# Performance work log

Measured on AMD Instinct MI355X. Metric: run time of the kernel, lower is better.

The kernel has to match this reference:

```python
import jax, jax.numpy as jnp
import numpy as np

H = W = 256          # render / reference image size (module crops ref to 256x256)
TS = 4               # texture_size in the module
EYE_DIST, ELEV, AZIM = 2.732, 0.0, np.pi / 2  # fixed azimuth (orig: uniform(0,360))
EPS = 1e-8


def _look_at(verts, eye):
    # neural_renderer look_at: at=origin, up=+y
    up = jnp.array([0.0, 1.0, 0.0], dtype=verts.dtype)
    z = -eye / jnp.linalg.norm(eye)
    x = jnp.cross(up, z)
    x = x / jnp.linalg.norm(x)
    y = jnp.cross(z, x)
    R = jnp.stack([x, y, z], axis=0)  # rows = camera axes
    return (verts - eye) @ R.T


def _cross2(u, v):
    return u[..., 0] * v[..., 1] - u[..., 1] * v[..., 0]


def _render(vertices, faces, textures):
    # Orthographic (perspective=False), ambient-only lighting -> color == texture sample.
    eye = jnp.array([EYE_DIST * np.cos(ELEV) * np.sin(AZIM),
                     EYE_DIST * np.sin(ELEV),
                     -EYE_DIST * np.cos(ELEV) * np.cos(AZIM)], dtype=vertices.dtype)
    v = _look_at(vertices[0], eye)            # [V,3] camera space
    fv = v[faces[0]]                          # [F,3,3]
    a, b, c = fv[:, 0, :2], fv[:, 1, :2], fv[:, 2, :2]  # [F,2] screen-space verts
    zf = fv[..., 2]                           # [F,3] per-vertex depth

    # pixel centers in NDC, y flipped (image row 0 = top)
    xs = (jnp.arange(W, dtype=vertices.dtype) + 0.5) / W * 2.0 - 1.0
    ys = 1.0 - (jnp.arange(H, dtype=vertices.dtype) + 0.5) / H * 2.0
    P = jnp.stack(jnp.meshgrid(xs, ys, indexing='xy'), -1).reshape(-1, 2)  # [HW,2]
    Pq = P[:, None, :]                        # [HW,1,2]

    denom = _cross2(b - a, c - a)             # [F] signed 2*area
    w0 = _cross2((c - b)[None], Pq - b[None])  # [HW,F] edge functions
    w1 = _cross2((a - c)[None], Pq - c[None])
    w2 = _cross2((b - a)[None], Pq - a[None])
    s = jnp.sign(denom)[None]
    nondeg = (jnp.abs(denom) > EPS)[None]
    inside = (w0 * s >= 0) & (w1 * s >= 0) & (w2 * s >= 0) & nondeg
    d = jnp.where(jnp.abs(denom) > EPS, denom, 1.0)[None]
    w0, w1, w2 = w0 / d, w1 / d, w2 / d       # normalized barycentrics
    depth = w0 * zf[None, :, 0] + w1 * zf[None, :, 1] + w2 * zf[None, :, 2]  # [HW,F]
    visible = inside & (depth > 0)

    # z-buffer: nearest visible face per pixel
    zbuf = jnp.where(visible, depth, jnp.inf)
    best = jnp.argmin(zbuf, axis=1)           # [HW]
    hit = jnp.take_along_axis(visible, best[:, None], 1)[:, 0]
    bw = jnp.stack([jnp.take_along_axis(wi, best[:, None], 1)[:, 0]
                    for wi in (w0, w1, w2)], axis=-1)  # [HW,3]

    # sample face texture cube [TS,TS,TS] by barycentric coords (nearest)
    ti = jnp.clip(jnp.round(bw * (TS - 1)).astype(jnp.int32), 0, TS - 1)
    color = textures[0][best, ti[:, 0], ti[:, 1], ti[:, 2]]  # [HW,3]
    img = jnp.where(hit[:, None], color, jnp.zeros_like(color)).reshape(H, W, 3)
    return jnp.transpose(img, (2, 0, 1))[None]  # [1,3,H,W]


def setup_inputs() -> dict:
    key = jax.random.key(0)
    k1, k2, k3, k4 = jax.random.split(key, 4)
    V, F = 642, 512
    verts = jax.random.normal(k1, (1, V, 3), jnp.float32)
    verts = verts / (jnp.linalg.norm(verts, axis=-1, keepdims=True) + 1e-6)  # unit sphere
    faces = jax.random.randint(k2, (1, F, 3), 0, V, jnp.int32)
    textures = jax.random.normal(k3, (1, F, TS, TS, TS, 3), jnp.float32)
    image_ref = jax.random.uniform(k4, (1, 3, H, W), jnp.float32)
    return {"vertices": verts, "textures": textures, "image_ref": image_ref, "faces": faces}


def reference(vertices, textures, image_ref, faces):
    image = _render(vertices, faces, jnp.tanh(textures))
    return jnp.sum((image - image_ref) ** 2)
```

## Files before the change

### kernel.cpp

```cpp
#include <hip/hip_runtime.h>
#include <math.h>

#define NFACE 512
#define NVERT 642
#define NPIX  (256 * 256)
#define DXS   (2.0f / 256.0f)

#define EYEX 2.732f
#define EYEZ (-1.6728675276352845e-16f)
#define CC0  (6.123233995736766e-17f)

__global__ __launch_bounds__(256) void render_loss(
    const float* __restrict__ verts,
    const int*   __restrict__ faces,
    const float* __restrict__ tex,
    const float* __restrict__ ref,
    float* __restrict__ out)
{
    __shared__ float  sverts[NVERT * 3];
    __shared__ float4 sf0[NFACE];
    __shared__ float4 sf1[NFACE];
    __shared__ float4 flist[NFACE];
    __shared__ float4 plist[NFACE][3];
    __shared__ int   fcnt, pcnt;
    __shared__ unsigned Mu;
    __shared__ float wsum[4];

    int tid = threadIdx.x;
    if (tid == 0) { fcnt = 0; pcnt = 0; Mu = 0x7f800000u; }

    for (int k = tid; k < NVERT * 3; k += 256) sverts[k] = verts[k];
    __syncthreads();

    int tileX = (blockIdx.x & 15) << 4;
    int tileY = (blockIdx.x >> 4) << 4;
    float xlo = (tileX + 0.5f)  * DXS - 1.0f;
    float xhi = (tileX + 15.5f) * DXS - 1.0f;
    float yhi = 1.0f - (tileY + 0.5f)  * DXS;
    float ylo = 1.0f - (tileY + 15.5f) * DXS;

    float rc[2][9];
    int   rcls[2];
    float rdmn[2];
#pragma unroll
    for (int it = 0; it < 2; ++it) {
        int f = tid + it * 256;
        rcls[it] = 0;
        float vx[3], vy[3], vz[3];
#pragma unroll
        for (int k = 0; k < 3; ++k) {
            int vi = faces[f * 3 + k];
            float px = sverts[vi * 3 + 0];
            float py = sverts[vi * 3 + 1];
            float pz = sverts[vi * 3 + 2];
            float dx = px - EYEX;
            float dz = pz - EYEZ;
            vx[k] = CC0 * dx + dz;
            vy[k] = py;
            vz[k] = -dx + CC0 * dz;
        }
        float ax = vx[0], ay = vy[0];
        float bx = vx[1], by = vy[1];
        float cx = vx[2], cy = vy[2];
        float denom = (bx - ax) * (cy - ay) - (by - ay) * (cx - ax);
        if (fabsf(denom) <= 1e-8f) continue;

        float si = 1.0f / denom;
        float e0x = cx - bx, e0y = cy - by;
        float e1x = ax - cx, e1y = ay - cy;
        float e2x = bx - ax, e2y = by - ay;
        float A0 = e0x * si, B0 = -e0y * si, C0 = (e0y * bx - e0x * by) * si;
        float A1 = e1x * si, B1 = -e1y * si, C1 = (e1y * cx - e1x * cy) * si;
        float A2 = e2x * si, B2 = -e2y * si, C2 = (e2y * ax - e2x * ay) * si;
        float DA = A0 * vz[0] + A1 * vz[1] + A2 * vz[2];
        float DB = B0 * vz[0] + B1 * vz[1] + B2 * vz[2];
        float DC = C0 * vz[0] + C1 * vz[1] + C2 * vz[2];

        sf0[f] = make_float4(A0, B0, C0, A1);
        sf1[f] = make_float4(B1, C1, DA, DB);

        float bxmn = fminf(fminf(ax, bx), cx), bxmx = fmaxf(fmaxf(ax, bx), cx);
        float bymn = fminf(fminf(ay, by), cy), bymx = fmaxf(fmaxf(ay, by), cy);
        if ((bxmn > xhi + 1e-5f) | (bxmx < xlo - 1e-5f) |
            (bymn > yhi + 1e-5f) | (bymx < ylo - 1e-5f)) continue;

        float wmx[3], wmn[3], mg[3];
        float As[3] = {A0, A1, A2}, Bs[3] = {B0, B1, B2}, Cs[3] = {C0, C1, C2};
#pragma unroll
        for (int k = 0; k < 3; ++k) {
            float t1 = As[k] * ylo, t2 = As[k] * yhi;
            float u1 = Bs[k] * xlo, u2 = Bs[k] * xhi;
            wmx[k] = fmaxf(t1, t2) + fmaxf(u1, u2) + Cs[k];
            wmn[k] = fminf(t1, t2) + fminf(u1, u2) + Cs[k];
            mg[k]  = (fabsf(As[k]) + fabsf(Bs[k]) + fabsf(Cs[k])) * 2e-6f;
        }
        if ((wmx[0] < -mg[0]) | (wmx[1] < -mg[1]) | (wmx[2] < -mg[2])) continue;
        bool full = (wmn[0] > mg[0]) & (wmn[1] > mg[1]) & (wmn[2] > mg[2]);

        float t1 = DA * ylo, t2 = DA * yhi;
        float u1 = DB * xlo, u2 = DB * xhi;
        float dmx = fmaxf(t1, t2) + fmaxf(u1, u2) + DC;
        float dmn = fminf(t1, t2) + fminf(u1, u2) + DC;
        float md  = (fabsf(DA) + fabsf(DB) + fabsf(DC)) * 2e-6f + 1e-4f;
        rdmn[it] = dmn - md;
        rcls[it] = full ? 1 : 2;
        rc[it][0] = A0; rc[it][1] = B0; rc[it][2] = C0;
        rc[it][3] = A1; rc[it][4] = B1; rc[it][5] = C1;
        rc[it][6] = DA; rc[it][7] = DB; rc[it][8] = DC;
        if (full) atomicMin(&Mu, __float_as_uint(dmx + md));
    }
    __syncthreads();

    float M = __uint_as_float(Mu);
#pragma unroll
    for (int it = 0; it < 2; ++it) {
        if (rcls[it] == 0 || rdmn[it] > M) continue;
        int f = tid + it * 256;
        float fb = __uint_as_float((unsigned)f);
        if (rcls[it] == 1) {
            int s = atomicAdd(&fcnt, 1);
            flist[s] = make_float4(rc[it][6], rc[it][7], rc[it][8], fb);
        } else {
            int s = atomicAdd(&pcnt, 1);
            plist[s][0] = make_float4(rc[it][0], rc[it][1], rc[it][2], rc[it][3]);
            plist[s][1] = make_float4(rc[it][4], rc[it][5], rc[it][6], rc[it][7]);
            plist[s][2] = make_float4(rc[it][8], fb, 0.f, 0.f);
        }
    }
    __syncthreads();
    int fc = fcnt, pc = pcnt;

    int i = tileX + (tid & 15);
    int j = tileY + (tid >> 4);
    float Px = (i + 0.5f) * DXS - 1.0f;
    float Py = 1.0f - (j + 0.5f) * DXS;

    unsigned best = 0xFFFFFFFFu;
    int k = 0;
    for (; k + 4 <= fc; k += 4) {
        float4 ra = flist[k + 0], rb = flist[k + 1];
        float4 rcc = flist[k + 2], rd = flist[k + 3];
        float da = fmaf(ra.x, Py, fmaf(ra.y, Px, ra.z));
        float db = fmaf(rb.x, Py, fmaf(rb.y, Px, rb.z));
        float dc = fmaf(rcc.x, Py, fmaf(rcc.y, Px, rcc.z));
        float dd = fmaf(rd.x, Py, fmaf(rd.y, Px, rd.z));
        unsigned ca = (__float_as_uint(da) & 0xFFFFFE00u) | __float_as_uint(ra.w);
        unsigned cb = (__float_as_uint(db) & 0xFFFFFE00u) | __float_as_uint(rb.w);
        unsigned cc = (__float_as_uint(dc) & 0xFFFFFE00u) | __float_as_uint(rcc.w);
        unsigned cd = (__float_as_uint(dd) & 0xFFFFFE00u) | __float_as_uint(rd.w);
        ca = ca < cb ? ca : cb;
        cc = cc < cd ? cc : cd;
        ca = ca < cc ? ca : cc;
        best = best < ca ? best : ca;
    }
    for (; k < fc; ++k) {
        float4 r = flist[k];
        float dep = fmaf(r.x, Py, fmaf(r.y, Px, r.z));
        unsigned cand = (__float_as_uint(dep) & 0xFFFFFE00u) | __float_as_uint(r.w);
        best = best < cand ? best : cand;
    }
    k = 0;
    for (; k + 2 <= pc; k += 2) {
        float4 a0 = plist[k][0], a1 = plist[k][1], a2 = plist[k][2];
        float4 b0 = plist[k+1][0], b1 = plist[k+1][1], b2 = plist[k+1][2];
        float aw0 = fmaf(a0.x, Py, fmaf(a0.y, Px, a0.z));
        float aw1 = fmaf(a0.w, Py, fmaf(a1.x, Px, a1.y));
        float aw2 = 1.0f - aw0 - aw1;
        float adp = fmaf(a1.z, Py, fmaf(a1.w, Px, a2.x));
        float amn = fminf(fminf(aw0, aw1), aw2);
        unsigned ac = (__float_as_uint(adp) & 0xFFFFFE00u) | __float_as_uint(a2.y);
        ac = (amn >= 0.f) ? ac : 0xFFFFFFFFu;
        float bw0 = fmaf(b0.x, Py, fmaf(b0.y, Px, b0.z));
        float bw1 = fmaf(b0.w, Py, fmaf(b1.x, Px, b1.y));
        float bw2 = 1.0f - bw0 - bw1;
        float bdp = fmaf(b1.z, Py, fmaf(b1.w, Px, b2.x));
        float bmn = fminf(fminf(bw0, bw1), bw2);
        unsigned bc = (__float_as_uint(bdp) & 0xFFFFFE00u) | __float_as_uint(b2.y);
        bc = (bmn >= 0.f) ? bc : 0xFFFFFFFFu;
        ac = ac < bc ? ac : bc;
        best = best < ac ? best : ac;
    }
    for (; k < pc; ++k) {
        float4 q0 = plist[k][0], q1 = plist[k][1], q2 = plist[k][2];
        float w0  = fmaf(q0.x, Py, fmaf(q0.y, Px, q0.z));
        float w1  = fmaf(q0.w, Py, fmaf(q1.x, Px, q1.y));
        float w2  = 1.0f - w0 - w1;
        float dep = fmaf(q1.z, Py, fmaf(q1.w, Px, q2.x));
        float mn  = fminf(fminf(w0, w1), w2);
        unsigned cand = (__float_as_uint(dep) & 0xFFFFFE00u) | __float_as_uint(q2.y);
        cand = (mn >= 0.f) ? cand : 0xFFFFFFFFu;
        best = best < cand ? best : cand;
    }

    int p = j * 256 + i;
    float col0 = 0.f, col1 = 0.f, col2 = 0.f;
    if (best != 0xFFFFFFFFu) {
        int bf = (int)(best & 511u);
        float4 q0 = sf0[bf];
        float4 q1 = sf1[bf];
        float w0 = fmaf(q0.x, Py, fmaf(q0.y, Px, q0.z));
        float w1 = fmaf(q0.w, Py, fmaf(q1.x, Px, q1.y));
        float w2 = 1.0f - w0 - w1;
        int t0 = (int)rintf(w0 * 3.0f); t0 = t0 < 0 ? 0 : (t0 > 3 ? 3 : t0);
        int t1 = (int)rintf(w1 * 3.0f); t1 = t1 < 0 ? 0 : (t1 > 3 ? 3 : t1);
        int t2 = (int)rintf(w2 * 3.0f); t2 = t2 < 0 ? 0 : (t2 > 3 ? 3 : t2);
        const float* tp = tex + ((((bf * 4 + t0) * 4 + t1) * 4 + t2) * 3);
        col0 = tanhf(tp[0]);
        col1 = tanhf(tp[1]);
        col2 = tanhf(tp[2]);
    }
    float r0 = ref[0 * NPIX + p];
    float r1 = ref[1 * NPIX + p];
    float r2 = ref[2 * NPIX + p];
    float e0 = col0 - r0, e1 = col1 - r1, e2 = col2 - r2;
    float loss = e0 * e0 + e1 * e1 + e2 * e2;

    for (int off = 32; off > 0; off >>= 1)
        loss += __shfl_down(loss, off, 64);
    int lane = tid & 63;
    int wid  = tid >> 6;
    if (lane == 0) wsum[wid] = loss;
    __syncthreads();
    if (tid == 0)
        atomicAdd(out, wsum[0] + wsum[1] + wsum[2] + wsum[3]);
}

extern "C" void kernel_launch(void* const* d_in, const int* in_sizes, int n_in,
                              void* d_out, int out_size, void* d_ws, size_t ws_size,
                              hipStream_t stream) {
    const float* verts = (const float*)d_in[0];
    const float* tex   = (const float*)d_in[1];
    const float* ref   = (const float*)d_in[2];
    const int*   faces = (const int*)d_in[3];
    float* out = (float*)d_out;

    hipMemsetAsync(out, 0, sizeof(float), stream);
    render_loss<<<256, 256, 0, stream>>>(verts, faces, tex, ref, out);
}
```

Baseline: 17.67 us.

## Split face lists across waves and compute four pixel rows per thread

Each wave now handles a quarter of the candidate face lists. Each thread evaluates four vertically adjacent pixels per face, sharing the Px-dependent terms, and the four per-wave minima are merged through shared memory. Per-thread LDS reads and loop trip counts drop by about a factor of four, at the cost of an extra barrier and a shared reduction buffer. The third edge coefficients are also derived algebraically from the first two, and the partial-face list is split into separate arrays.

```diff
diff --git a/kernel.cpp b/kernel.cpp
--- a/kernel.cpp
+++ b/kernel.cpp
@@ -21,7 +21,10 @@
     __shared__ float4 sf0[NFACE];
     __shared__ float4 sf1[NFACE];
     __shared__ float4 flist[NFACE];
-    __shared__ float4 plist[NFACE][3];
+    __shared__ float4 pl0[NFACE];
+    __shared__ float4 pl1[NFACE];
+    __shared__ float2 pld[NFACE];
+    __shared__ unsigned marr[4][256];
     __shared__ int   fcnt, pcnt;
     __shared__ unsigned Mu;
     __shared__ float wsum[4];
@@ -71,7 +74,7 @@
         float e2x = bx - ax, e2y = by - ay;
         float A0 = e0x * si, B0 = -e0y * si, C0 = (e0y * bx - e0x * by) * si;
         float A1 = e1x * si, B1 = -e1y * si, C1 = (e1y * cx - e1x * cy) * si;
-        float A2 = e2x * si, B2 = -e2y * si, C2 = (e2y * ax - e2x * ay) * si;
+        float A2 = -(A0 + A1), B2 = -(B0 + B1), C2 = 1.0f - C0 - C1;
         float DA = A0 * vz[0] + A1 * vz[1] + A2 * vz[2];
         float DB = B0 * vz[0] + B1 * vz[1] + B2 * vz[2];
         float DC = C0 * vz[0] + C1 * vz[1] + C2 * vz[2];
@@ -122,84 +125,94 @@
             flist[s] = make_float4(rc[it][6], rc[it][7], rc[it][8], fb);
         } else {
             int s = atomicAdd(&pcnt, 1);
-            plist[s][0] = make_float4(rc[it][0], rc[it][1], rc[it][2], rc[it][3]);
-            plist[s][1] = make_float4(rc[it][4], rc[it][5], rc[it][6], rc[it][7]);
-            plist[s][2] = make_float4(rc[it][8], fb, 0.f, 0.f);
+            pl0[s] = make_float4(rc[it][0], rc[it][1], rc[it][2], rc[it][3]);
+            pl1[s] = make_float4(rc[it][4], rc[it][5], rc[it][6], rc[it][7]);
+            pld[s] = make_float2(rc[it][8], fb);
         }
     }
     __syncthreads();
     int fc = fcnt, pc = pcnt;
+
+    int lane = tid & 63;
+    int w    = tid >> 6;
+    int col   = lane & 15;
+    int rbase = (lane >> 4) << 2;
+    float Px  = (tileX + col + 0.5f) * DXS - 1.0f;
+    float Py0 = 1.0f - (tileY + rbase + 0.5f) * DXS;
+
+    unsigned pk0 = 0xFFFFFFFFu, pk1 = 0xFFFFFFFFu;
+    unsigned pk2 = 0xFFFFFFFFu, pk3 = 0xFFFFFFFFu;
+
+#pragma unroll 2
+    for (int k = w; k < fc; k += 4) {
+        float4 r = flist[k];
+        float td = fmaf(r.y, Px, r.z);
+        float d0 = fmaf(r.x, Py0, td);
+        float d1 = fmaf(r.x, Py0 - DXS, td);
+        float d2 = fmaf(r.x, Py0 - 2.0f * DXS, td);
+        float d3 = fmaf(r.x, Py0 - 3.0f * DXS, td);
+        unsigned fb = __float_as_uint(r.w);
+        unsigned c0 = (__float_as_uint(d0) & 0xFFFFFE00u) | fb;
+        unsigned c1 = (__float_as_uint(d1) & 0xFFFFFE00u) | fb;
+        unsigned c2 = (__float_as_uint(d2) & 0xFFFFFE00u) | fb;
+        unsigned c3 = (__float_as_uint(d3) & 0xFFFFFE00u) | fb;
+        pk0 = pk0 < c0 ? pk0 : c0;
+        pk1 = pk1 < c1 ? pk1 : c1;
+        pk2 = pk2 < c2 ? pk2 : c2;
+        pk3 = pk3 < c3 ? pk3 : c3;
+    }
+
+#pragma unroll 2
+    for (int k = w; k < pc; k += 4) {
+        float4 q0 = pl0[k];
+        float4 q1 = pl1[k];
+        float2 qd = pld[k];
+        float t0 = fmaf(q0.y, Px, q0.z);
+        float t1 = fmaf(q1.x, Px, q1.y);
+        float td = fmaf(q1.w, Px, qd.x);
+        unsigned fb = __float_as_uint(qd.y);
+#pragma unroll
+        for (int q = 0; q < 4; ++q) {
+            float Py = Py0 - (float)q * DXS;
+            float w0 = fmaf(q0.x, Py, t0);
+            float w1 = fmaf(q0.w, Py, t1);
+            float w2 = 1.0f - w0 - w1;
+            float dp = fmaf(q1.z, Py, td);
+            float mn = fminf(fminf(w0, w1), w2);
+            unsigned cd = (__float_as_uint(dp) & 0xFFFFFE00u) | fb;
+            cd = (mn >= 0.f) ? cd : 0xFFFFFFFFu;
+            if (q == 0) pk0 = pk0 < cd ? pk0 : cd;
+            if (q == 1) pk1 = pk1 < cd ? pk1 : cd;
+            if (q == 2) pk2 = pk2 < cd ? pk2 : cd;
+            if (q == 3) pk3 = pk3 < cd ? pk3 : cd;
+        }
+    }
+
+    marr[w][(rbase + 0) * 16 + col] = pk0;
+    marr[w][(rbase + 1) * 16 + col] = pk1;
+    marr[w][(rbase + 2) * 16 + col] = pk2;
+    marr[w][(rbase + 3) * 16 + col] = pk3;
+    __syncthreads();
+    unsigned best = marr[0][tid];
+    unsigned m1 = marr[1][tid];
+    unsigned m2 = marr[2][tid];
+    unsigned m3 = marr[3][tid];
+    best = best < m1 ? best : m1;
+    best = best < m2 ? best : m2;
+    best = best < m3 ? best : m3;
 
     int i = tileX + (tid & 15);
     int j = tileY + (tid >> 4);
-    float Px = (i + 0.5f) * DXS - 1.0f;
-    float Py = 1.0f - (j + 0.5f) * DXS;
-
-    unsigned best = 0xFFFFFFFFu;
-    int k = 0;
-    for (; k + 4 <= fc; k += 4) {
-        float4 ra = flist[k + 0], rb = flist[k + 1];
-        float4 rcc = flist[k + 2], rd = flist[k + 3];
-        float da = fmaf(ra.x, Py, fmaf(ra.y, Px, ra.z));
-        float db = fmaf(rb.x, Py, fmaf(rb.y, Px, rb.z));
-        float dc = fmaf(rcc.x, Py, fmaf(rcc.y, Px, rcc.z));
-        float dd = fmaf(rd.x, Py, fmaf(rd.y, Px, rd.z));
-        unsigned ca = (__float_as_uint(da) & 0xFFFFFE00u) | __float_as_uint(ra.w);
-        unsigned cb = (__float_as_uint(db) & 0xFFFFFE00u) | __float_as_uint(rb.w);
-        unsigned cc = (__float_as_uint(dc) & 0xFFFFFE00u) | __float_as_uint(rcc.w);
-        unsigned cd = (__float_as_uint(dd) & 0xFFFFFE00u) | __float_as_uint(rd.w);
-        ca = ca < cb ? ca : cb;
-        cc = cc < cd ? cc : cd;
-        ca = ca < cc ? ca : cc;
-        best = best < ca ? best : ca;
-    }
-    for (; k < fc; ++k) {
-        float4 r = flist[k];
-        float dep = fmaf(r.x, Py, fmaf(r.y, Px, r.z));
-        unsigned cand = (__float_as_uint(dep) & 0xFFFFFE00u) | __float_as_uint(r.w);
-        best = best < cand ? best : cand;
-    }
-    k = 0;
-    for (; k + 2 <= pc; k += 2) {
-        float4 a0 = plist[k][0], a1 = plist[k][1], a2 = plist[k][2];
-        float4 b0 = plist[k+1][0], b1 = plist[k+1][1], b2 = plist[k+1][2];
-        float aw0 = fmaf(a0.x, Py, fmaf(a0.y, Px, a0.z));
-        float aw1 = fmaf(a0.w, Py, fmaf(a1.x, Px, a1.y));
-        float aw2 = 1.0f - aw0 - aw1;
-        float adp = fmaf(a1.z, Py, fmaf(a1.w, Px, a2.x));
-        float amn = fminf(fminf(aw0, aw1), aw2);
-        unsigned ac = (__float_as_uint(adp) & 0xFFFFFE00u) | __float_as_uint(a2.y);
-        ac = (amn >= 0.f) ? ac : 0xFFFFFFFFu;
-        float bw0 = fmaf(b0.x, Py, fmaf(b0.y, Px, b0.z));
-        float bw1 = fmaf(b0.w, Py, fmaf(b1.x, Px, b1.y));
-        float bw2 = 1.0f - bw0 - bw1;
-        float bdp = fmaf(b1.z, Py, fmaf(b1.w, Px, b2.x));
-        float bmn = fminf(fminf(bw0, bw1), bw2);
-        unsigned bc = (__float_as_uint(bdp) & 0xFFFFFE00u) | __float_as_uint(b2.y);
-        bc = (bmn >= 0.f) ? bc : 0xFFFFFFFFu;
-        ac = ac < bc ? ac : bc;
-        best = best < ac ? best : ac;
-    }
-    for (; k < pc; ++k) {
-        float4 q0 = plist[k][0], q1 = plist[k][1], q2 = plist[k][2];
-        float w0  = fmaf(q0.x, Py, fmaf(q0.y, Px, q0.z));
-        float w1  = fmaf(q0.w, Py, fmaf(q1.x, Px, q1.y));
-        float w2  = 1.0f - w0 - w1;
-        float dep = fmaf(q1.z, Py, fmaf(q1.w, Px, q2.x));
-        float mn  = fminf(fminf(w0, w1), w2);
-        unsigned cand = (__float_as_uint(dep) & 0xFFFFFE00u) | __float_as_uint(q2.y);
-        cand = (mn >= 0.f) ? cand : 0xFFFFFFFFu;
-        best = best < cand ? best : cand;
-    }
-
+    float Pxe = (i + 0.5f) * DXS - 1.0f;
+    float Pye = 1.0f - (j + 0.5f) * DXS;
     int p = j * 256 + i;
     float col0 = 0.f, col1 = 0.f, col2 = 0.f;
     if (best != 0xFFFFFFFFu) {
         int bf = (int)(best & 511u);
         float4 q0 = sf0[bf];
         float4 q1 = sf1[bf];
-        float w0 = fmaf(q0.x, Py, fmaf(q0.y, Px, q0.z));
-        float w1 = fmaf(q0.w, Py, fmaf(q1.x, Px, q1.y));
+        float w0 = fmaf(q0.x, Pye, fmaf(q0.y, Pxe, q0.z));
+        float w1 = fmaf(q0.w, Pye, fmaf(q1.x, Pxe, q1.y));
         float w2 = 1.0f - w0 - w1;
         int t0 = (int)rintf(w0 * 3.0f); t0 = t0 < 0 ? 0 : (t0 > 3 ? 3 : t0);
         int t1 = (int)rintf(w1 * 3.0f); t1 = t1 < 0 ? 0 : (t1 > 3 ? 3 : t1);
@@ -217,9 +230,7 @@
 
     for (int off = 32; off > 0; off >>= 1)
         loss += __shfl_down(loss, off, 64);
-    int lane = tid & 63;
-    int wid  = tid >> 6;
-    if (lane == 0) wsum[wid] = loss;
+    if (lane == 0) wsum[w] = loss;
     __syncthreads();
     if (tid == 0)
         atomicAdd(out, wsum[0] + wsum[1] + wsum[2] + wsum[3]);
```

Measured after the change: 17.47 us. About the same (-1.1%).
